# Kernel tuning notes

Measured on AMD Instinct MI355X. Metric: run time of the kernel, lower is better.

Reference implementation:

```python
import jax, jax.numpy as jnp
import numpy as np

L, D, H, N, R = 4, 256, 512, 16, 8  # layers, d_model, hidden=2*d_model, state_dim, dt_rank
OUT_LEN, IN_DIM = 96, 32
EPS = 1e-5


def _layernorm(v, g, b):
    m = jnp.mean(v, axis=-1, keepdims=True)
    var = jnp.mean((v - m) ** 2, axis=-1, keepdims=True)
    return (v - m) / jnp.sqrt(var + EPS) * g + b


def _pos_encoding(T, d):
    pos = jnp.arange(T, dtype=jnp.float32)[:, None]
    div = jnp.exp(jnp.arange(0, d, 2, dtype=jnp.float32) * (-np.log(10000.0) / d))
    pe = jnp.zeros((T, d), dtype=jnp.float32)
    pe = pe.at[:, 0::2].set(jnp.sin(pos * div))
    pe = pe.at[:, 1::2].set(jnp.cos(pos * div))
    return pe


def setup_inputs() -> dict:
    key = jax.random.key(0)
    ks = jax.random.split(key, 20)
    inp = {
        "x": jax.random.normal(ks[0], (8, 1024, IN_DIM), dtype=jnp.float32),
        "emb_w": jax.random.normal(ks[1], (D, IN_DIM), dtype=jnp.float32) * 0.1,
        "emb_b": jnp.zeros((D,), dtype=jnp.float32),
        "norm_g": jnp.ones((L, D), dtype=jnp.float32),
        "norm_b": jnp.zeros((L, D), dtype=jnp.float32),
        "in_w": jax.random.normal(ks[2], (L, H, D), dtype=jnp.float32) * (1.0 / np.sqrt(D)),
        "conv_w": jax.random.normal(ks[3], (L, H, 1, 3), dtype=jnp.float32) * 0.5,
        "A_p": jax.random.normal(ks[4], (L, H, N), dtype=jnp.float32) * 0.01,
        "D_p": jnp.ones((L, H), dtype=jnp.float32),
        "dt1_w": jax.random.normal(ks[5], (L, R, H), dtype=jnp.float32) * (1.0 / np.sqrt(H)),
        "dt1_b": jnp.zeros((L, R), dtype=jnp.float32),
        "dt2_w": jax.random.normal(ks[6], (L, H, R), dtype=jnp.float32) * (1.0 / np.sqrt(R)),
        "dt2_b": jnp.zeros((L, H), dtype=jnp.float32),
        "out_w": jax.random.normal(ks[7], (L, D, H), dtype=jnp.float32) * (1.0 / np.sqrt(H)),
        "final_g": jnp.ones((D,), dtype=jnp.float32),
        "final_b": jnp.zeros((D,), dtype=jnp.float32),
        "head1_w": jax.random.normal(ks[8], (D, D), dtype=jnp.float32) * (1.0 / np.sqrt(D)),
        "head1_b": jnp.zeros((D,), dtype=jnp.float32),
        "head2_w": jax.random.normal(ks[9], (OUT_LEN, D), dtype=jnp.float32) * (1.0 / np.sqrt(D)),
        "head2_b": jnp.zeros((OUT_LEN,), dtype=jnp.float32),
    }
    return inp


def _mamba_block(h, g, b, in_w, conv_w, A_p, D_p, dt1_w, dt1_b, dt2_w, dt2_b, out_w):
    res = h
    v = _layernorm(h, g, b)            # [B,T,D]
    v = jnp.einsum('btd,hd->bth', v, in_w)  # [B,T,H]
    # depthwise conv1d, kernel 3, padding 1, groups=H
    vc = jnp.transpose(v, (0, 2, 1))   # [B,H,T]
    vc = jax.lax.conv_general_dilated(vc, conv_w, window_strides=(1,),
                                      padding=[(1, 1)], feature_group_count=H,
                                      dimension_numbers=('NCH', 'OIH', 'NCH'))
    v = jnp.transpose(jax.nn.silu(vc), (0, 2, 1))  # [B,T,H]
    dt = jax.nn.relu(jnp.einsum('bth,rh->btr', v, dt1_w) + dt1_b)
    dt = jnp.einsum('btr,hr->bth', dt, dt2_w) + dt2_b
    dt = jax.nn.softplus(dt)           # [B,T,H]
    A = -jnp.exp(A_p)                  # [H,N]
    safe_A = jnp.where(jnp.abs(A) < 1e-5, jnp.ones_like(A), A)

    B_sz = v.shape[0]
    state0 = jnp.zeros((B_sz, H, N), dtype=v.dtype)

    def step(state, inp):
        x_t, dt_t = inp  # [B,H] each
        dA = A * dt_t[..., None]            # [B,H,N]
        discA = jnp.exp(dA)
        discB = (discA - 1.0) / safe_A * dt_t[..., None]
        state = discA * state + discB * x_t[..., None]
        y = jnp.einsum('bhn,hn->bh', state, A_p) + D_p * x_t
        return state, y

    xs = (jnp.transpose(v, (1, 0, 2)), jnp.transpose(dt, (1, 0, 2)))  # [T,B,H]
    _, ys = jax.lax.scan(step, state0, xs)
    y = jnp.transpose(ys, (1, 0, 2))   # [B,T,H]
    return res + jnp.einsum('bth,dh->btd', y, out_w)


def reference(x, emb_w, emb_b, norm_g, norm_b, in_w, conv_w, A_p, D_p,
              dt1_w, dt1_b, dt2_w, dt2_b, out_w, final_g, final_b,
              head1_w, head1_b, head2_w, head2_b):
    h = jnp.einsum('bti,di->btd', x, emb_w) + emb_b  # [B,T,D]
    h = h + _pos_encoding(h.shape[1], D)[None]
    for l in range(L):
        h = _mamba_block(h, norm_g[l], norm_b[l], in_w[l], conv_w[l], A_p[l],
                         D_p[l], dt1_w[l], dt1_b[l], dt2_w[l], dt2_b[l], out_w[l])
    h = _layernorm(h, final_g, final_b)
    h = h[:, -1, :]                    # last token [B,D]
    h = jax.nn.silu(h @ head1_w.T + head1_b)
    return h @ head2_w.T + head2_b     # [B, OUT_LEN]
```

## Files before the change

kernel.cpp:

```cpp
#include <hip/hip_runtime.h>
#include <hip/hip_bf16.h>
#include <math.h>

#define BB 8
#define TT 1024
#define DD 256
#define HH 512
#define NN 16
#define RR 8
#define OUT_LEN 96
#define IN_DIM 32
#define MM (BB*TT)

#define SC 16
#define CC (TT/SC)

typedef unsigned short u16;
typedef unsigned int u32;
typedef __attribute__((ext_vector_type(8))) short short8;
typedef __attribute__((ext_vector_type(8))) unsigned short u16x8;
typedef __attribute__((ext_vector_type(4))) float float4v;

__device__ __forceinline__ u16 f2bf(float f) {
    __hip_bfloat16 h = __float2bfloat16(f);
    return *(u16*)&h;
}
__device__ __forceinline__ float bf2f(u16 u) {
    u32 v = ((u32)u) << 16;
    return *(float*)&v;
}

#define GLD_LDS16(src, dst) __builtin_amdgcn_global_load_lds( \
    (const __attribute__((address_space(1))) void*)(src),     \
    (__attribute__((address_space(3))) void*)(dst), 16, 0, 0)

#define SBAR()   asm volatile("s_barrier" ::: "memory")
#define VMCNT0() asm volatile("s_waitcnt vmcnt(0)" ::: "memory")
#define VMCNT4() asm volatile("s_waitcnt vmcnt(4)" ::: "memory")
#define VMCNT6() asm volatile("s_waitcnt vmcnt(6)" ::: "memory")
#define VMCNT8() asm volatile("s_waitcnt vmcnt(8)" ::: "memory")

__global__ __launch_bounds__(256) void embed_ln_cvt_kernel(
    const float* __restrict__ x, const float* __restrict__ emb_w,
    const float* __restrict__ emb_b,
    const float* __restrict__ g, const float* __restrict__ b,
    float* __restrict__ h, u16* __restrict__ lnout,
    const float* __restrict__ w_in, u16* __restrict__ wbf_in,
    const float* __restrict__ w_out, u16* __restrict__ wbf_out, int nw)
{
    int bid = blockIdx.x;
    if (bid >= MM) {
        int i = (bid - MM) * 256 + threadIdx.x;
        if (i < nw) wbf_in[i] = f2bf(w_in[i]);
        else        wbf_out[i - nw] = f2bf(w_out[i - nw]);
        return;
    }

    int bt = bid;
    int d  = threadIdx.x;
    int t  = bt & (TT - 1);

    __shared__ float xs[IN_DIM];
    __shared__ float red[4], red2[4];
    if (threadIdx.x < IN_DIM) xs[threadIdx.x] = x[bt * IN_DIM + threadIdx.x];
    __syncthreads();

    const float* w = emb_w + d * IN_DIM;
    float acc = emb_b[d];
#pragma unroll
    for (int i = 0; i < IN_DIM; i++) acc = fmaf(xs[i], w[i], acc);

    int i2 = d & ~1;
    float div = __expf(-(float)i2 * 0.0359778918f);
    float arg = (float)t * div;
    float pe = (d & 1) ? __cosf(arg) : __sinf(arg);
    float val = acc + pe;
    h[bt * DD + d] = val;

    float s = val;
#pragma unroll
    for (int o = 32; o > 0; o >>= 1) s += __shfl_down(s, o);
    int lane = d & 63, wave = d >> 6;
    if (lane == 0) red[wave] = s;
    __syncthreads();
    float mean = (red[0] + red[1] + red[2] + red[3]) * (1.0f / DD);

    float c = val - mean;
    float s2 = c * c;
#pragma unroll
    for (int o = 32; o > 0; o >>= 1) s2 += __shfl_down(s2, o);
    if (lane == 0) red2[wave] = s2;
    __syncthreads();
    float var = (red2[0] + red2[1] + red2[2] + red2[3]) * (1.0f / DD);

    lnout[bt * DD + d] = f2bf(c * rsqrtf(var + 1e-5f) * g[d] + b[d]);
}

template<int BM, int BN, int OUT_BF16>
__global__ __launch_bounds__(256) void gemm_bf16(
    const u16* __restrict__ A, const u16* __restrict__ B,
    void* __restrict__ Cv, int M, int N, int K, int addC)
{
    constexpr int BK = 64;
    constexpr int MT = BM / 32;
    constexpr int NT = BN / 32;
    static_assert(BM == 128 && BN == 64, "vmcnt count assumes 6 loads/thread");

    __shared__ __align__(16) u16 Al[2][8][BM][8];
    __shared__ __align__(16) u16 Bl[2][8][BN][8];

    const int tid = threadIdx.x;
    const int bm = blockIdx.y * BM;
    const int bn = blockIdx.x * BN;
    const int wid = tid >> 6, lane = tid & 63;
    const int wm = wid >> 1, wn = wid & 1;
    const int lq = lane >> 4, lm = lane & 15;

    float4v acc[MT][NT];
#pragma unroll
    for (int i = 0; i < MT; i++)
#pragma unroll
        for (int j = 0; j < NT; j++) acc[i][j] = (float4v){0.f, 0.f, 0.f, 0.f};

#pragma unroll
    for (int it = 0; it < (8 * BM) / 256; it++) {
        int c = it * 256 + tid;
        int q = c / BM, row = c % BM;
        GLD_LDS16(A + (size_t)(bm + row) * K + q * 8, &Al[0][q][row][0]);
    }
#pragma unroll
    for (int it = 0; it < (8 * BN) / 256; it++) {
        int c = it * 256 + tid;
        int q = c / BN, row = c % BN;
        GLD_LDS16(B + (size_t)(bn + row) * K + q * 8, &Bl[0][q][row][0]);
    }

    const int nt = K / BK;
    int cur = 0;
    for (int i = 0; i < nt; i++) {
        if (i + 1 < nt) {
            int nxt = cur ^ 1;
            int k1 = (i + 1) * BK;
#pragma unroll
            for (int it = 0; it < (8 * BM) / 256; it++) {
                int c = it * 256 + tid;
                int q = c / BM, row = c % BM;
                GLD_LDS16(A + (size_t)(bm + row) * K + k1 + q * 8, &Al[nxt][q][row][0]);
            }
#pragma unroll
            for (int it = 0; it < (8 * BN) / 256; it++) {
                int c = it * 256 + tid;
                int q = c / BN, row = c % BN;
                GLD_LDS16(B + (size_t)(bn + row) * K + k1 + q * 8, &Bl[nxt][q][row][0]);
            }
            VMCNT6();
        } else {
            VMCNT0();
        }
        SBAR();

        short8 af[2][MT], bf[2][NT];
#pragma unroll
        for (int kk = 0; kk < 2; kk++) {
#pragma unroll
            for (int mt = 0; mt < MT; mt++)
                af[kk][mt] = *(const short8*)&Al[cur][kk * 4 + lq][wm * (BM / 2) + mt * 16 + lm][0];
#pragma unroll
            for (int nt2 = 0; nt2 < NT; nt2++)
                bf[kk][nt2] = *(const short8*)&Bl[cur][kk * 4 + lq][wn * (BN / 2) + nt2 * 16 + lm][0];
        }

#pragma unroll
        for (int kk = 0; kk < 2; kk++)
#pragma unroll
            for (int mt = 0; mt < MT; mt++)
#pragma unroll
                for (int nt2 = 0; nt2 < NT; nt2++)
                    acc[mt][nt2] = __builtin_amdgcn_mfma_f32_16x16x32_bf16(
                        af[kk][mt], bf[kk][nt2], acc[mt][nt2], 0, 0, 0);
        SBAR();
        cur ^= 1;
    }

#pragma unroll
    for (int mt = 0; mt < MT; mt++)
#pragma unroll
        for (int nt2 = 0; nt2 < NT; nt2++) {
            int row0 = bm + wm * (BM / 2) + mt * 16 + lq * 4;
            int col  = bn + wn * (BN / 2) + nt2 * 16 + lm;
#pragma unroll
            for (int r = 0; r < 4; r++) {
                float vv = acc[mt][nt2][r];
                if (OUT_BF16) {
                    ((u16*)Cv)[(size_t)(row0 + r) * N + col] = f2bf(vv);
                } else {
                    float* cp = (float*)Cv + (size_t)(row0 + r) * N + col;
                    if (addC) vv += *cp;
                    *cp = vv;
                }
            }
        }
}

__device__ __forceinline__ float softplus_f(float s) {
    return (s > 20.0f) ? s : __logf(1.0f + __expf(s));
}

__global__ __launch_bounds__(512, 4) void conv_scan1(
    const u16* __restrict__ vbf, const float* __restrict__ cwg,
    const float* __restrict__ w1g, const float* __restrict__ b1g,
    const float* __restrict__ dt2_w, const float* __restrict__ dt2_b,
    const float* __restrict__ A_p, const float* __restrict__ D_p,
    u16* __restrict__ vsb, float* __restrict__ dtr,
    u16* __restrict__ Lst, float* __restrict__ sdt,
    u16* __restrict__ ybf)
{
    const int c = blockIdx.x;
    const int b = blockIdx.y;
    const int tid = threadIdx.x;
    const int wave = tid >> 6, lane = tid & 63;
    const int h0 = lane * 8;

    __shared__ float w1s[RR * 2 * 256];
    __shared__ u16   a_lds[SC][HH];
    __shared__ float ds[SC * RR];

#pragma unroll
    for (int i = 0; i < 2; i++) {
        int rci = wave + i * 8;
        int r = rci >> 1, jc = rci & 1;
        float4 wv = *(const float4*)(w1g + r * HH + lane * 8 + jc * 4);
        *(float4*)&w1s[rci * 256 + lane * 4] = wv;
    }
    __syncthreads();

    const float* wp = cwg + h0 * 3;
#pragma unroll
    for (int i = 0; i < 2; i++) {
        int tr = wave + i * 8;
        int t  = c * SC + tr;
        size_t m = (size_t)b * TT + t;

        const u16* vrow = vbf + m * HH + h0;
        u16x8 x0 = *(const u16x8*)vrow;
        u16x8 xm = (t > 0)      ? *(const u16x8*)(vrow - HH) : (u16x8)(0);
        u16x8 xp = (t < TT - 1) ? *(const u16x8*)(vrow + HH) : (u16x8)(0);

        float a[8];
        u16x8 o;
#pragma unroll
        for (int j = 0; j < 8; j++) {
            float s = wp[j * 3] * bf2f(xm[j]);
            s = fmaf(wp[j * 3 + 1], bf2f(x0[j]), s);
            s = fmaf(wp[j * 3 + 2], bf2f(xp[j]), s);
            s = s / (1.0f + __expf(-s));
            a[j] = s;
            o[j] = f2bf(s);
        }
        *(u16x8*)(vsb + m * HH + h0) = o;
        *(u16x8*)&a_lds[tr][h0]      = o;

        float acc[RR];
#pragma unroll
        for (int r = 0; r < RR; r++) {
            float4 wlo = *(const float4*)&w1s[(r * 2 + 0) * 256 + lane * 4];
            float4 whi = *(const float4*)&w1s[(r * 2 + 1) * 256 + lane * 4];
            float s = a[0] * wlo.x;
            s = fmaf(a[1], wlo.y, s);
            s = fmaf(a[2], wlo.z, s);
            s = fmaf(a[3], wlo.w, s);
            s = fmaf(a[4], whi.x, s);
            s = fmaf(a[5], whi.y, s);
            s = fmaf(a[6], whi.z, s);
            s = fmaf(a[7], whi.w, s);
            acc[r] = s;
        }
#pragma unroll
        for (int r = 0; r < RR; r++) {
#pragma unroll
            for (int o2 = 1; o2 < 64; o2 <<= 1) acc[r] += __shfl_xor(acc[r], o2);
        }
        if (lane == 0) {
#pragma unroll
            for (int r = 0; r < RR; r++) acc[r] = fmaxf(acc[r] + b1g[r], 0.0f);
            *(float4*)(dtr + m * RR)     = make_float4(acc[0], acc[1], acc[2], acc[3]);
            *(float4*)(dtr + m * RR + 4) = make_float4(acc[4], acc[5], acc[6], acc[7]);
#pragma unroll
            for (int r = 0; r < RR; r++) ds[tr * RR + r] = acc[r];
        }
    }
    __syncthreads();

    const int h = tid;
    float A2[NN], invA[NN], Apr[NN], st[NN];
    const float* ap = A_p + h * NN;
#pragma unroll
    for (int n = 0; n < NN; n++) {
        float apv = ap[n];
        Apr[n] = apv;
        float av = -__expf(apv);
        A2[n] = av * 1.44269504f;
        invA[n] = 1.0f / av;
        st[n] = 0.0f;
    }
    float w2[RR];
#pragma unroll
    for (int r = 0; r < RR; r++) w2[r] = dt2_w[h * RR + r];
    float b2 = dt2_b[h];
    float Dp = D_p[h];

    u16* ybase = ybf + ((size_t)b * TT + (size_t)c * SC) * HH + h;

    float xv = bf2f(a_lds[0][h]);
    float s_dt = 0.0f;
#pragma unroll 2
    for (int t = 0; t < SC; t++) {
        float xn = (t + 1 < SC) ? bf2f(a_lds[t + 1][h]) : 0.0f;
        float s = b2;
#pragma unroll
        for (int r = 0; r < RR; r++) s = fmaf(ds[t * RR + r], w2[r], s);
        float dt = softplus_f(s);
        s_dt += dt;
        float dtx = dt * xv;
        float accY = Dp * xv;
#pragma unroll
        for (int n = 0; n < NN; n++) {
            float e = __builtin_amdgcn_exp2f(A2[n] * dt);
            float u = invA[n] * dtx;
            st[n] = fmaf(e, st[n] + u, -u);
            accY = fmaf(st[n], Apr[n], accY);
        }
        ybase[(size_t)t * HH] = f2bf(accY);
        xv = xn;
    }

    size_t base = (((size_t)c * BB + b) * HH + h) * NN;
    u16x8 lo, hi;
#pragma unroll
    for (int n = 0; n < 8; n++) { lo[n] = f2bf(st[n]); hi[n] = f2bf(st[n + 8]); }
    *(u16x8*)(Lst + base)     = lo;
    *(u16x8*)(Lst + base + 8) = hi;
    sdt[((size_t)c * BB + b) * HH + h] = s_dt;
}

__global__ __launch_bounds__(256) void scan_carry_par(
    const float* __restrict__ A_p, const float* __restrict__ sdt,
    u16* __restrict__ Lst)
{
    int gw   = (blockIdx.x << 2) | (threadIdx.x >> 6);
    int lane = threadIdx.x & 63;
    int b = gw >> 9;
    int h = gw & 511;

    size_t sidx = ((size_t)lane * BB + b) * HH + h;
    float sd = sdt[sidx];
    const float* ap = A_p + h * NN;
    u16x8 Llo = *(const u16x8*)(Lst + sidx * NN);
    u16x8 Lhi = *(const u16x8*)(Lst + sidx * NN + 8);
    u16x8 Elo, Ehi;
#pragma unroll
    for (int n = 0; n < NN; n++) {
        float An = -__expf(ap[n]);
        float p  = __expf(An * sd);
        float lv = bf2f((n < 8) ? Llo[n] : Lhi[n - 8]);
#pragma unroll
        for (int d2 = 1; d2 < 64; d2 <<= 1) {
            float pp = __shfl_up(p, d2);
            float pl = __shfl_up(lv, d2);
            if (lane >= d2) { lv = fmaf(pl, p, lv); p = pp * p; }
        }
        float E = __shfl_up(lv, 1);
        if (lane == 0) E = 0.0f;
        if (n < 8) Elo[n] = f2bf(E); else Ehi[n - 8] = f2bf(E);
    }
    *(u16x8*)(Lst + sidx * NN)     = Elo;
    *(u16x8*)(Lst + sidx * NN + 8) = Ehi;
}

__global__ __launch_bounds__(512) void scan2_gemm2_ln(
    const u16* __restrict__ ybf, const float* __restrict__ dtr,
    const float* __restrict__ dt2_w, const float* __restrict__ dt2_b,
    const float* __restrict__ A_p,
    const u16* __restrict__ carry,
    const u16* __restrict__ B,
    float* __restrict__ h,
    const float* __restrict__ g, const float* __restrict__ bb,
    u16* __restrict__ lnout, int doLN,
    const float* __restrict__ w1h, const float* __restrict__ b1h,
    const float* __restrict__ w2h, const float* __restrict__ b2h,
    float* __restrict__ outp, int doHead)
{
    const int bid = blockIdx.x;
    const int b   = bid >> 5;
    const int tb  = bid & 31;
    const int t0  = tb * 32;
    const int c0  = tb * 2;
    const int bm  = bid * 32;

    const int tid = threadIdx.x;
    const int wid = tid >> 6;
    const int lane = tid & 63;
    const int lq = lane >> 4, lm = lane & 15;
    const int wm = wid >> 2;
    const int wn = wid & 3;

    __shared__ __align__(16) u16 Yl[32 * 512];
    __shared__ __align__(16) u16 Bl[3][8][256][8];
    __shared__ float ds[32 * RR];
    __shared__ float rs[4][32], qs[4][32];
    __shared__ float hn[DD], sl1[DD];

#pragma unroll
    for (int pt = 0; pt < 2; pt++) {
#pragma unroll
        for (int it = 0; it < 4; it++) {
            int cth = it * 512 + tid;
            int q = cth >> 8, row = cth & 255;
            GLD_LDS16(B + (size_t)row * 512 + pt * 64 + q * 8, &Bl[pt][q][row][0]);
        }
    }

    const int hh = tid;

    float K0[NN], K1[NN];
    float A2[NN];
    {
        size_t cb0 = (((size_t)(c0 + 0) * BB + b) * HH + hh) * NN;
        size_t cb1 = (((size_t)(c0 + 1) * BB + b) * HH + hh) * NN;
        u16x8 l0 = *(const u16x8*)(carry + cb0);
        u16x8 h0 = *(const u16x8*)(carry + cb0 + 8);
        u16x8 l1 = *(const u16x8*)(carry + cb1);
        u16x8 h1 = *(const u16x8*)(carry + cb1 + 8);
        const float* ap = A_p + hh * NN;
#pragma unroll
        for (int n = 0; n < NN; n++) {
            float apv = ap[n];
            float av = -__expf(apv);
            A2[n] = av * 1.44269504f;
            float c0v = bf2f((n < 8) ? l0[n] : h0[n - 8]);
            float c1v = bf2f((n < 8) ? l1[n] : h1[n - 8]);
            K0[n] = apv * c0v;
            K1[n] = apv * c1v;
        }
    }

    if (tid < 256) {
        int tr = tid >> 3, r = tid & 7;
        ds[tid] = dtr[((size_t)b * TT + t0 + tr) * RR + r];
    }

    float w2[RR];
#pragma unroll
    for (int r = 0; r < RR; r++) w2[r] = dt2_w[hh * RR + r];
    float b2 = dt2_b[hh];
    __syncthreads();

    const u16* yb0 = ybf + ((size_t)b * TT + (size_t)(c0 + 0) * SC) * HH + hh;
    const u16* yb1 = ybf + ((size_t)b * TT + (size_t)(c0 + 1) * SC) * HH + hh;
    float cd0 = 0.0f, cd1 = 0.0f;
#pragma unroll
    for (int t = 0; t < SC; t++) {
        float s0 = b2, s1 = b2;
#pragma unroll
        for (int r = 0; r < RR; r++) {
            s0 = fmaf(ds[t * RR + r], w2[r], s0);
            s1 = fmaf(ds[(SC + t) * RR + r], w2[r], s1);
        }
        cd0 += softplus_f(s0);
        cd1 += softplus_f(s1);
        float yl0 = bf2f(yb0[(size_t)t * HH]);
        float yl1 = bf2f(yb1[(size_t)t * HH]);
        float corr0 = 0.0f, corr1 = 0.0f;
#pragma unroll
        for (int n = 0; n < NN; n++) {
            corr0 = fmaf(K0[n], __builtin_amdgcn_exp2f(A2[n] * cd0), corr0);
            corr1 = fmaf(K1[n], __builtin_amdgcn_exp2f(A2[n] * cd1), corr1);
        }
        Yl[t * 512 + (hh ^ ((t & 7) << 3))] = f2bf(yl0 + corr0);
        int tr1 = SC + t;
        Yl[tr1 * 512 + (hh ^ ((tr1 & 7) << 3))] = f2bf(yl1 + corr1);
    }
    __syncthreads();

    float4v acc4[4];
#pragma unroll
    for (int j = 0; j < 4; j++) acc4[j] = (float4v){0.f, 0.f, 0.f, 0.f};

    for (int i = 0; i < 8; i++) {
        if (i + 2 < 8) {
            int nb = (i + 2) % 3;
            int k1 = (i + 2) * 64;
#pragma unroll
            for (int it = 0; it < 4; it++) {
                int cth = it * 512 + tid;
                int q = cth >> 8, row = cth & 255;
                GLD_LDS16(B + (size_t)row * 512 + k1 + q * 8, &Bl[nb][q][row][0]);
            }
            VMCNT8();
        } else if (i + 1 < 8) {
            VMCNT4();
        } else {
            VMCNT0();
        }
        SBAR();

        int cur = i % 3;
        int k0 = i * 64;
        short8 af[2], bf[2][4];
#pragma unroll
        for (int kk = 0; kk < 2; kk++) {
            int row = wm * 16 + lm;
            int kg  = (k0 >> 3) + kk * 4 + lq;
            af[kk] = *(const short8*)&Yl[row * 512 + ((kg ^ (row & 7)) << 3)];
#pragma unroll
            for (int nt = 0; nt < 4; nt++)
                bf[kk][nt] = *(const short8*)&Bl[cur][kk * 4 + lq][wn * 64 + nt * 16 + lm][0];
        }
#pragma unroll
        for (int kk = 0; kk < 2; kk++)
#pragma unroll
            for (int nt = 0; nt < 4; nt++)
                acc4[nt] = __builtin_amdgcn_mfma_f32_16x16x32_bf16(
                    af[kk], bf[kk][nt], acc4[nt], 0, 0, 0);
        SBAR();
    }

    float val[4][4];
    float s1[4] = {0.f, 0.f, 0.f, 0.f}, s2[4] = {0.f, 0.f, 0.f, 0.f};
#pragma unroll
    for (int r = 0; r < 4; r++) {
        int row = bm + wm * 16 + lq * 4 + r;
#pragma unroll
        for (int nt = 0; nt < 4; nt++) {
            int col = wn * 64 + nt * 16 + lm;
            float v = acc4[nt][r] + h[(size_t)row * DD + col];
            val[r][nt] = v;
            s1[r] += v;
            s2[r] = fmaf(v, v, s2[r]);
            h[(size_t)row * DD + col] = v;
        }
    }
#pragma unroll
    for (int r = 0; r < 4; r++) {
#pragma unroll
        for (int o = 1; o < 16; o <<= 1) {
            s1[r] += __shfl_xor(s1[r], o);
            s2[r] += __shfl_xor(s2[r], o);
        }
    }
    if (lm == 0) {
#pragma unroll
        for (int r = 0; r < 4; r++) {
            rs[wn][wm * 16 + lq * 4 + r] = s1[r];
            qs[wn][wm * 16 + lq * 4 + r] = s2[r];
        }
    }
    __syncthreads();

    if (doLN) {
#pragma unroll
        for (int r = 0; r < 4; r++) {
            int i = wm * 16 + lq * 4 + r;
            int row = bm + i;
            float mean = (rs[0][i] + rs[1][i] + rs[2][i] + rs[3][i]) * (1.0f / DD);
            float var  = (qs[0][i] + qs[1][i] + qs[2][i] + qs[3][i]) * (1.0f / DD) - mean * mean;
            float rstd = rsqrtf(var + 1e-5f);
#pragma unroll
            for (int nt = 0; nt < 4; nt++) {
                int col = wn * 64 + nt * 16 + lm;
                lnout[(size_t)row * DD + col] =
                    f2bf((val[r][nt] - mean) * rstd * g[col] + bb[col]);
            }
        }
    }

    if (doHead && tb == 31) {
        const int i31 = 31;
        float mean = (rs[0][i31] + rs[1][i31] + rs[2][i31] + rs[3][i31]) * (1.0f / DD);
        float var  = (qs[0][i31] + qs[1][i31] + qs[2][i31] + qs[3][i31]) * (1.0f / DD) - mean * mean;
        float rstd = rsqrtf(var + 1e-5f);
        const size_t row = (size_t)bm + 31;

        if (tid < DD) {
            float v = h[row * DD + tid];
            hn[tid] = (v - mean) * rstd * g[tid] + bb[tid];
        }
        __syncthreads();

        if (tid < DD) {
            float a1 = b1h[tid];
            const float* w1r = w1h + tid * DD;
#pragma unroll 8
            for (int k = 0; k < DD; k++) a1 = fmaf(hn[k], w1r[k], a1);
            sl1[tid] = a1 / (1.0f + __expf(-a1));
        }
        __syncthreads();

        if (tid < OUT_LEN) {
            float a2 = b2h[tid];
            const float* w2r = w2h + tid * DD;
#pragma unroll 8
            for (int k = 0; k < DD; k++) a2 = fmaf(sl1[k], w2r[k], a2);
            outp[b * OUT_LEN + tid] = a2;
        }
    }
}

extern "C" void kernel_launch(void* const* d_in, const int* in_sizes, int n_in,
                              void* d_out, int out_size, void* d_ws, size_t ws_size,
                              hipStream_t stream)
{
    (void)in_sizes; (void)n_in; (void)out_size; (void)ws_size;

    const float* x       = (const float*)d_in[0];
    const float* emb_w   = (const float*)d_in[1];
    const float* emb_b   = (const float*)d_in[2];
    const float* norm_g  = (const float*)d_in[3];
    const float* norm_b  = (const float*)d_in[4];
    const float* in_w    = (const float*)d_in[5];
    const float* conv_w  = (const float*)d_in[6];
    const float* A_p     = (const float*)d_in[7];
    const float* D_p     = (const float*)d_in[8];
    const float* dt1_w   = (const float*)d_in[9];
    const float* dt1_b   = (const float*)d_in[10];
    const float* dt2_w   = (const float*)d_in[11];
    const float* dt2_b   = (const float*)d_in[12];
    const float* out_w   = (const float*)d_in[13];
    const float* final_g = (const float*)d_in[14];
    const float* final_b = (const float*)d_in[15];
    const float* head1_w = (const float*)d_in[16];
    const float* head1_b = (const float*)d_in[17];
    const float* head2_w = (const float*)d_in[18];
    const float* head2_b = (const float*)d_in[19];
    float* outp = (float*)d_out;

    char* ws = (char*)d_ws;
    float* h     = (float*)ws;                ws += (size_t)MM * DD * 4;
    u16*   vbf   = (u16*)ws;                  ws += (size_t)MM * HH * 2;
    u16*   vsb   = (u16*)ws;                  ws += (size_t)MM * HH * 2;
    u16*   ybf   = (u16*)ws;                  ws += (size_t)MM * HH * 2;
    u16*   lnbuf = (u16*)ws;                  ws += (size_t)MM * DD * 2;
    float* dtr   = (float*)ws;                ws += (size_t)MM * RR * 4;
    u16*   Lst   = (u16*)ws;                  ws += (size_t)CC * BB * HH * NN * 2;
    float* sdt   = (float*)ws;                ws += (size_t)CC * BB * HH * 4;
    u16*   wbf_in  = (u16*)ws;                ws += (size_t)4 * HH * DD * 2;
    u16*   wbf_out = (u16*)ws;                ws += (size_t)4 * DD * HH * 2;

    const int NW = 4 * HH * DD;
    embed_ln_cvt_kernel<<<MM + (2 * NW) / 256, 256, 0, stream>>>(
        x, emb_w, emb_b, norm_g, norm_b, h, lnbuf,
        in_w, wbf_in, out_w, wbf_out, NW);

    for (int l = 0; l < 4; l++) {
        gemm_bf16<128, 64, 1><<<dim3(HH / 64, MM / 128), 256, 0, stream>>>(
            lnbuf, wbf_in + (size_t)l * HH * DD, vbf, MM, HH, DD, 0);

        conv_scan1<<<dim3(CC, BB), 512, 0, stream>>>(
            vbf, conv_w + (size_t)l * HH * 3,
            dt1_w + (size_t)l * RR * HH, dt1_b + l * RR,
            dt2_w + (size_t)l * HH * RR, dt2_b + l * HH,
            A_p + (size_t)l * HH * NN, D_p + l * HH,
            vsb, dtr, Lst, sdt, ybf);

        scan_carry_par<<<(BB * HH) / 4, 256, 0, stream>>>(
            A_p + (size_t)l * HH * NN, sdt, Lst);

        const float* g_next = (l < 3) ? (norm_g + (l + 1) * DD) : final_g;
        const float* b_next = (l < 3) ? (norm_b + (l + 1) * DD) : final_b;
        scan2_gemm2_ln<<<MM / 32, 512, 0, stream>>>(
            ybf, dtr, dt2_w + (size_t)l * HH * RR, dt2_b + l * HH,
            A_p + (size_t)l * HH * NN,
            Lst, wbf_out + (size_t)l * DD * HH,
            h, g_next, b_next, lnbuf, (l < 3) ? 1 : 0,
            head1_w, head1_b, head2_w, head2_b, outp, (l == 3) ? 1 : 0);
    }
}
```

Measured before the change: 453.1 us.

## Read out_w B-fragments directly from global and drop unused vsb write

The second GEMM in scan2_gemm2_ln no longer stages the out_w tile through a triple-buffered LDS ring with global_load_lds and barriers. Each wave now loads its B fragments straight from global memory (which should hit in L2/L1, since every block reuses the same weight) and issues the MFMAs without per-step barriers. This also frees a large LDS allocation, which may raise occupancy. Separately, conv_scan1 stops writing the vsb buffer, which nothing read, saving a full activation-sized store per layer. The risk is higher global-load latency per MFMA with no explicit prefetching.

```diff
diff --git a/kernel.cpp b/kernel.cpp
--- a/kernel.cpp
+++ b/kernel.cpp
@@ -36,9 +36,7 @@
 
 #define SBAR()   asm volatile("s_barrier" ::: "memory")
 #define VMCNT0() asm volatile("s_waitcnt vmcnt(0)" ::: "memory")
-#define VMCNT4() asm volatile("s_waitcnt vmcnt(4)" ::: "memory")
 #define VMCNT6() asm volatile("s_waitcnt vmcnt(6)" ::: "memory")
-#define VMCNT8() asm volatile("s_waitcnt vmcnt(8)" ::: "memory")
 
 __global__ __launch_bounds__(256) void embed_ln_cvt_kernel(
     const float* __restrict__ x, const float* __restrict__ emb_w,
@@ -211,7 +209,7 @@
     const float* __restrict__ w1g, const float* __restrict__ b1g,
     const float* __restrict__ dt2_w, const float* __restrict__ dt2_b,
     const float* __restrict__ A_p, const float* __restrict__ D_p,
-    u16* __restrict__ vsb, float* __restrict__ dtr,
+    float* __restrict__ dtr,
     u16* __restrict__ Lst, float* __restrict__ sdt,
     u16* __restrict__ ybf)
 {
@@ -257,8 +255,7 @@
             a[j] = s;
             o[j] = f2bf(s);
         }
-        *(u16x8*)(vsb + m * HH + h0) = o;
-        *(u16x8*)&a_lds[tr][h0]      = o;
+        *(u16x8*)&a_lds[tr][h0] = o;
 
         float acc[RR];
 #pragma unroll
@@ -405,20 +402,9 @@
     const int wn = wid & 3;
 
     __shared__ __align__(16) u16 Yl[32 * 512];
-    __shared__ __align__(16) u16 Bl[3][8][256][8];
     __shared__ float ds[32 * RR];
     __shared__ float rs[4][32], qs[4][32];
     __shared__ float hn[DD], sl1[DD];
-
-#pragma unroll
-    for (int pt = 0; pt < 2; pt++) {
-#pragma unroll
-        for (int it = 0; it < 4; it++) {
-            int cth = it * 512 + tid;
-            int q = cth >> 8, row = cth & 255;
-            GLD_LDS16(B + (size_t)row * 512 + pt * 64 + q * 8, &Bl[pt][q][row][0]);
-        }
-    }
 
     const int hh = tid;
 
@@ -486,43 +472,22 @@
 #pragma unroll
     for (int j = 0; j < 4; j++) acc4[j] = (float4v){0.f, 0.f, 0.f, 0.f};
 
+    const int arow = wm * 16 + lm;
+#pragma unroll
     for (int i = 0; i < 8; i++) {
-        if (i + 2 < 8) {
-            int nb = (i + 2) % 3;
-            int k1 = (i + 2) * 64;
-#pragma unroll
-            for (int it = 0; it < 4; it++) {
-                int cth = it * 512 + tid;
-                int q = cth >> 8, row = cth & 255;
-                GLD_LDS16(B + (size_t)row * 512 + k1 + q * 8, &Bl[nb][q][row][0]);
+        int k0 = i * 64;
+#pragma unroll
+        for (int kk = 0; kk < 2; kk++) {
+            int kg = (k0 >> 3) + kk * 4 + lq;
+            short8 af = *(const short8*)&Yl[arow * 512 + ((kg ^ (arow & 7)) << 3)];
+#pragma unroll
+            for (int nt = 0; nt < 4; nt++) {
+                int brow = wn * 64 + nt * 16 + lm;
+                short8 bf = *(const short8*)(B + (size_t)brow * 512 + k0 + (kk * 4 + lq) * 8);
+                acc4[nt] = __builtin_amdgcn_mfma_f32_16x16x32_bf16(
+                    af, bf, acc4[nt], 0, 0, 0);
             }
-            VMCNT8();
-        } else if (i + 1 < 8) {
-            VMCNT4();
-        } else {
-            VMCNT0();
-        }
-        SBAR();
-
-        int cur = i % 3;
-        int k0 = i * 64;
-        short8 af[2], bf[2][4];
-#pragma unroll
-        for (int kk = 0; kk < 2; kk++) {
-            int row = wm * 16 + lm;
-            int kg  = (k0 >> 3) + kk * 4 + lq;
-            af[kk] = *(const short8*)&Yl[row * 512 + ((kg ^ (row & 7)) << 3)];
-#pragma unroll
-            for (int nt = 0; nt < 4; nt++)
-                bf[kk][nt] = *(const short8*)&Bl[cur][kk * 4 + lq][wn * 64 + nt * 16 + lm][0];
-        }
-#pragma unroll
-        for (int kk = 0; kk < 2; kk++)
-#pragma unroll
-            for (int nt = 0; nt < 4; nt++)
-                acc4[nt] = __builtin_amdgcn_mfma_f32_16x16x32_bf16(
-                    af[kk], bf[kk][nt], acc4[nt], 0, 0, 0);
-        SBAR();
+        }
     }
 
     float val[4][4];
@@ -637,7 +602,6 @@
     char* ws = (char*)d_ws;
     float* h     = (float*)ws;                ws += (size_t)MM * DD * 4;
     u16*   vbf   = (u16*)ws;                  ws += (size_t)MM * HH * 2;
-    u16*   vsb   = (u16*)ws;                  ws += (size_t)MM * HH * 2;
     u16*   ybf   = (u16*)ws;                  ws += (size_t)MM * HH * 2;
     u16*   lnbuf = (u16*)ws;                  ws += (size_t)MM * DD * 2;
     float* dtr   = (float*)ws;                ws += (size_t)MM * RR * 4;
@@ -660,7 +624,7 @@
             dt1_w + (size_t)l * RR * HH, dt1_b + l * RR,
             dt2_w + (size_t)l * HH * RR, dt2_b + l * HH,
             A_p + (size_t)l * HH * NN, D_p + l * HH,
-            vsb, dtr, Lst, sdt, ybf);
+            dtr, Lst, sdt, ybf);
 
         scan_carry_par<<<(BB * HH) / 4, 256, 0, stream>>>(
             A_p + (size_t)l * HH * NN, sdt, Lst);
```

Measured after the change: 479.8 us. +5.9%, slower.
